# Performance work log

Hardware: AMD Instinct MI355X
Metric: run time of the kernel (lower is better)

The kernel has to match this reference:

```python
import jax, jax.numpy as jnp
import numpy as np

NEG_INF = -9e15  # matches -9000000000000000.0 in torch code
ALPHA = 0.2      # LeakyReLU negative slope


def setup_inputs() -> dict:
    key = jax.random.key(0)
    k1, k2, k3, k4 = jax.random.split(key, 4)
    B, N, Fin, Fout = 8, 2048, 256, 256
    h = jax.random.normal(k1, (B, N, Fin), dtype=jnp.float32)
    adj = jax.random.randint(k2, (B, N, N), 0, 2, dtype=jnp.int32)
    W = jax.random.normal(k3, (Fin, Fout), dtype=jnp.float32) * 0.05
    a = jax.random.normal(k4, (2 * Fout, 1), dtype=jnp.float32) * 0.05
    return {"h": h, "adj": adj, "W": W, "a": a}


def reference(h, adj, W, a):
    # h: [B,N,Fin], adj: [B,N,N], W: [Fin,Fout], a: [2*Fout,1]
    Fout = W.shape[1]
    Wh = jnp.matmul(h, W)                       # [B,N,Fout]
    # Decompose concat-based additive score: e_ij = LReLU(a1.Wh_i + a2.Wh_j)
    a1 = a[:Fout, 0]                            # source-node part
    a2 = a[Fout:, 0]                            # target-node part
    s1 = jnp.einsum('bnf,f->bn', Wh, a1)        # [B,N]
    s2 = jnp.einsum('bnf,f->bn', Wh, a2)        # [B,N]
    e = jax.nn.leaky_relu(s1[:, :, None] + s2[:, None, :], negative_slope=ALPHA)  # [B,N,N]
    attn = jnp.where(adj > 0, e, NEG_INF)
    attn = jax.nn.softmax(attn, axis=2)          # masked softmax over neighbors
    # dropout omitted (deterministic eval-mode reference)
    h_prime = jnp.matmul(attn, Wh)               # [B,N,Fout]
    return h_prime
```

## Files before the change

### kernel.cpp

```cpp
#include <hip/hip_runtime.h>
#include <cstdint>

#define ALPHA 0.2f

constexpr int NB = 8;
constexpr int NN = 2048;
constexpr int NF = 256;

typedef __attribute__((ext_vector_type(8))) short bf16x8;
typedef __attribute__((ext_vector_type(4))) float f32x4;

__device__ __forceinline__ float bf2f(unsigned short u) {
    union { unsigned int i; float f; } v;
    v.i = ((unsigned int)u) << 16;
    return v.f;
}
__device__ __forceinline__ unsigned short f2bf(float f) {
    union { float f; unsigned int i; } v;
    v.f = f;
    v.i += 0x7fffu + ((v.i >> 16) & 1);
    return (unsigned short)(v.i >> 16);
}

__global__ __launch_bounds__(256) void k_wt(const float* __restrict__ W,
                                            unsigned short* __restrict__ WT,
                                            float* __restrict__ s1,
                                            float* __restrict__ s2) {
    const int t = threadIdx.x;
    const int gid = blockIdx.x * 256 + t;
    s1[gid] = 0.f;
    s2[gid] = 0.f;
    const int k = blockIdx.x * 4 + (t >> 6);
    const int f0 = (t & 63) * 4;
    const float4 w = *(const float4*)&W[k * NF + f0];
    WT[(f0 + 0) * NF + k] = f2bf(w.x);
    WT[(f0 + 1) * NF + k] = f2bf(w.y);
    WT[(f0 + 2) * NF + k] = f2bf(w.z);
    WT[(f0 + 3) * NF + k] = f2bf(w.w);
}

__global__ __launch_bounds__(256, 4) void k_wh(const float* __restrict__ h,
                                               const unsigned short* __restrict__ WT,
                                               const float* __restrict__ a,
                                               unsigned short* __restrict__ WhT,
                                               float* __restrict__ s1,
                                               float* __restrict__ s2) {
    __shared__ __align__(16) unsigned short As[64][72];
    __shared__ __align__(16) unsigned short Bs[64][72];
    const int tid = threadIdx.x;
    const int lane = tid & 63;
    const int l16 = lane & 15;
    const int quad = lane >> 4;
    const int wave = tid >> 6;
    const int row0 = (blockIdx.x >> 2) * 64;
    const int col0 = (blockIdx.x & 3) * 64;
    const int bb = row0 >> 11;
    const int n0 = row0 & (NN - 1);
    const int mb = (wave & 1) * 32;
    const int nb = (wave >> 1) * 32;

    f32x4 acc[2][2];
#pragma unroll
    for (int mf = 0; mf < 2; ++mf)
#pragma unroll
        for (int nf = 0; nf < 2; ++nf) acc[mf][nf] = (f32x4){0.f, 0.f, 0.f, 0.f};

    for (int k0 = 0; k0 < NF; k0 += 64) {
#pragma unroll
        for (int it = 0; it < 4; ++it) {
            const int q = tid + it * 256;
            const int r = q >> 4;
            const int k4 = (q & 15) * 4;
            const float4 v = *(const float4*)&h[(size_t)(row0 + r) * NF + k0 + k4];
            ushort4 o;
            o.x = f2bf(v.x); o.y = f2bf(v.y); o.z = f2bf(v.z); o.w = f2bf(v.w);
            *(ushort4*)&As[r][k4] = o;
        }
#pragma unroll
        for (int it = 0; it < 2; ++it) {
            const int q = tid + it * 256;
            const int f = q >> 3;
            const int k8 = (q & 7) * 8;
            *(uint4*)&Bs[f][k8] =
                *(const uint4*)&WT[(size_t)(col0 + f) * NF + k0 + k8];
        }
        __syncthreads();
#pragma unroll
        for (int ks = 0; ks < 64; ks += 32) {
            bf16x8 av[2], bv[2];
#pragma unroll
            for (int mf = 0; mf < 2; ++mf)
                av[mf] = *(const bf16x8*)&As[mb + mf * 16 + l16][ks + quad * 8];
#pragma unroll
            for (int nf = 0; nf < 2; ++nf)
                bv[nf] = *(const bf16x8*)&Bs[nb + nf * 16 + l16][ks + quad * 8];
#pragma unroll
            for (int mf = 0; mf < 2; ++mf)
#pragma unroll
                for (int nf = 0; nf < 2; ++nf)
                    acc[mf][nf] = __builtin_amdgcn_mfma_f32_16x16x32_bf16(
                        av[mf], bv[nf], acc[mf][nf], 0, 0, 0);
        }
        __syncthreads();
    }

#pragma unroll
    for (int mf = 0; mf < 2; ++mf) {
#pragma unroll
        for (int nf = 0; nf < 2; ++nf) {
            const size_t f = col0 + nb + nf * 16 + l16;
            const int nr = n0 + mb + mf * 16 + quad * 4;
            ushort4 o;
            o.x = f2bf(acc[mf][nf][0]);
            o.y = f2bf(acc[mf][nf][1]);
            o.z = f2bf(acc[mf][nf][2]);
            o.w = f2bf(acc[mf][nf][3]);
            *(ushort4*)&WhT[((size_t)bb * NF + f) * NN + nr] = o;
        }
    }

    float a1v[2], a2v[2];
#pragma unroll
    for (int nf = 0; nf < 2; ++nf) {
        const int f = col0 + nb + nf * 16 + l16;
        a1v[nf] = a[f];
        a2v[nf] = a[NF + f];
    }
#pragma unroll
    for (int mf = 0; mf < 2; ++mf) {
#pragma unroll
        for (int r = 0; r < 4; ++r) {
            float p1 = acc[mf][0][r] * a1v[0] + acc[mf][1][r] * a1v[1];
            float p2 = acc[mf][0][r] * a2v[0] + acc[mf][1][r] * a2v[1];
            p1 += __shfl_xor(p1, 1); p2 += __shfl_xor(p2, 1);
            p1 += __shfl_xor(p1, 2); p2 += __shfl_xor(p2, 2);
            p1 += __shfl_xor(p1, 4); p2 += __shfl_xor(p2, 4);
            p1 += __shfl_xor(p1, 8); p2 += __shfl_xor(p2, 8);
            if (l16 == 0) {
                const int n = n0 + mb + mf * 16 + quad * 4 + r;
                atomicAdd(&s1[bb * NN + n], p1);
                atomicAdd(&s2[bb * NN + n], p2);
            }
        }
    }
}

__global__ __launch_bounds__(256, 3) void k_attn(const unsigned short* __restrict__ WhT,
                                                 const int* __restrict__ adj,
                                                 const float* __restrict__ s1g,
                                                 const float* __restrict__ s2g,
                                                 float* __restrict__ out) {
    __shared__ __align__(16) unsigned short WhsT[256][72];
    __shared__ __align__(16) unsigned short Pb[32][72];
    __shared__ float s1_s[32];
    __shared__ float l_s[32];

    const int tid = threadIdx.x;
    const int lane = tid & 63;
    const int l16 = lane & 15;
    const int quad = lane >> 4;
    const int wave = tid >> 6;
    const int bb = blockIdx.x >> 6;
    const int i0 = (blockIdx.x & 63) * 32;

    if (tid < 32) {
        s1_s[tid] = s1g[bb * NN + i0 + tid];
        l_s[tid] = 0.f;
    }
    __syncthreads();

    f32x4 acc[2][4];
#pragma unroll
    for (int m = 0; m < 2; ++m)
#pragma unroll
        for (int nf = 0; nf < 4; ++nf) acc[m][nf] = (f32x4){0.f, 0.f, 0.f, 0.f};

    const size_t whtBase = (size_t)bb * NF * NN;
    const size_t adjBase = (size_t)bb * NN * NN;
    const float* s2b = s2g + bb * NN;

    const int whF = tid >> 3;
    const int whK = (tid & 7) * 8;
    const int pIr = tid >> 4;
    const int pKq = (tid & 15) * 4;

    const unsigned short* whP = &WhT[whtBase + (size_t)whF * NN + whK];
    const int* adjP0 = &adj[adjBase + (size_t)(i0 + pIr) * NN + pKq];
    const int* adjP1 = adjP0 + 16 * NN;
    const float* s2P = &s2b[pKq];

    uint4 w0, w1, w2, w3, w4, w5, w6, w7;
    int4 am0, am1;
    float4 sv0, sv1;

#define LOAD_TILE(J0)                                                         \
    do {                                                                      \
        const int j0_ = (J0);                                                 \
        w0 = *(const uint4*)&whP[(size_t)(0 * 32) * NN + j0_];                \
        w1 = *(const uint4*)&whP[(size_t)(1 * 32) * NN + j0_];                \
        w2 = *(const uint4*)&whP[(size_t)(2 * 32) * NN + j0_];                \
        w3 = *(const uint4*)&whP[(size_t)(3 * 32) * NN + j0_];                \
        w4 = *(const uint4*)&whP[(size_t)(4 * 32) * NN + j0_];                \
        w5 = *(const uint4*)&whP[(size_t)(5 * 32) * NN + j0_];                \
        w6 = *(const uint4*)&whP[(size_t)(6 * 32) * NN + j0_];                \
        w7 = *(const uint4*)&whP[(size_t)(7 * 32) * NN + j0_];                \
        am0 = *(const int4*)&adjP0[j0_];                                      \
        am1 = *(const int4*)&adjP1[j0_];                                      \
        sv0 = *(const float4*)&s2P[j0_];                                      \
        sv1 = sv0;                                                            \
    } while (0)

    LOAD_TILE(0);

    for (int t = 0; t < NN / 64; ++t) {
        *(uint4*)&WhsT[whF + 0 * 32][whK] = w0;
        *(uint4*)&WhsT[whF + 1 * 32][whK] = w1;
        *(uint4*)&WhsT[whF + 2 * 32][whK] = w2;
        *(uint4*)&WhsT[whF + 3 * 32][whK] = w3;
        *(uint4*)&WhsT[whF + 4 * 32][whK] = w4;
        *(uint4*)&WhsT[whF + 5 * 32][whK] = w5;
        *(uint4*)&WhsT[whF + 6 * 32][whK] = w6;
        *(uint4*)&WhsT[whF + 7 * 32][whK] = w7;
#pragma unroll
        for (int it = 0; it < 2; ++it) {
            const int ir = pIr + it * 16;
            const int4 av = it ? am1 : am0;
            const float4 s2v = it ? sv1 : sv0;
            const float s1v = s1_s[ir];
            float x0 = s1v + s2v.x, x1 = s1v + s2v.y;
            float x2 = s1v + s2v.z, x3 = s1v + s2v.w;
            x0 = x0 > 0.f ? x0 : ALPHA * x0;
            x1 = x1 > 0.f ? x1 : ALPHA * x1;
            x2 = x2 > 0.f ? x2 : ALPHA * x2;
            x3 = x3 > 0.f ? x3 : ALPHA * x3;
            const float p0 = av.x > 0 ? __expf(x0) : 0.f;
            const float p1 = av.y > 0 ? __expf(x1) : 0.f;
            const float p2 = av.z > 0 ? __expf(x2) : 0.f;
            const float p3 = av.w > 0 ? __expf(x3) : 0.f;
            uint2 pk;
            pk.x = (unsigned int)f2bf(p0) | ((unsigned int)f2bf(p1) << 16);
            pk.y = (unsigned int)f2bf(p2) | ((unsigned int)f2bf(p3) << 16);
            *(uint2*)&Pb[ir][pKq] = pk;
            float ps = (p0 + p1) + (p2 + p3);
            ps += __shfl_xor(ps, 8);
            ps += __shfl_xor(ps, 4);
            ps += __shfl_xor(ps, 2);
            ps += __shfl_xor(ps, 1);
            if ((tid & 15) == 0) l_s[ir] += ps;
        }
        __syncthreads();
        if (t + 1 < NN / 64) LOAD_TILE((t + 1) * 64);
        const int f0 = wave * 64;
#pragma unroll
        for (int k0 = 0; k0 < 64; k0 += 32) {
            bf16x8 af[2];
#pragma unroll
            for (int m = 0; m < 2; ++m)
                af[m] = *(const bf16x8*)&Pb[m * 16 + l16][k0 + quad * 8];
#pragma unroll
            for (int nf = 0; nf < 4; ++nf) {
                const bf16x8 bfr =
                    *(const bf16x8*)&WhsT[f0 + nf * 16 + l16][k0 + quad * 8];
#pragma unroll
                for (int m = 0; m < 2; ++m)
                    acc[m][nf] = __builtin_amdgcn_mfma_f32_16x16x32_bf16(
                        af[m], bfr, acc[m][nf], 0, 0, 0);
            }
        }
        __syncthreads();
    }
#undef LOAD_TILE

    if (tid < 32) l_s[tid] = 1.0f / l_s[tid];
    __syncthreads();

    const int f0 = wave * 64;
#pragma unroll
    for (int m = 0; m < 2; ++m) {
#pragma unroll
        for (int r = 0; r < 4; ++r) {
            const int row = m * 16 + quad * 4 + r;
            const float inv = l_s[row];
#pragma unroll
            for (int nf = 0; nf < 4; ++nf) {
                out[((size_t)bb * NN + i0 + row) * NF + f0 + nf * 16 + l16] =
                    acc[m][nf][r] * inv;
            }
        }
    }
}

extern "C" void kernel_launch(void* const* d_in, const int* in_sizes, int n_in,
                              void* d_out, int out_size, void* d_ws, size_t ws_size,
                              hipStream_t stream) {
    const float* h = (const float*)d_in[0];
    const int* adj = (const int*)d_in[1];
    const float* W = (const float*)d_in[2];
    const float* a = (const float*)d_in[3];
    float* out = (float*)d_out;

    unsigned short* WhT = (unsigned short*)d_ws;
    float* s1 = (float*)((char*)d_ws + (size_t)NB * NN * NF * sizeof(unsigned short));
    float* s2 = s1 + (size_t)NB * NN;
    unsigned short* WT = (unsigned short*)(s2 + (size_t)NB * NN);

    k_wt<<<dim3(64), dim3(256), 0, stream>>>(W, WT, s1, s2);
    k_wh<<<dim3((NB * NN / 64) * (NF / 64)), dim3(256), 0, stream>>>(h, WT, a, WhT, s1, s2);
    k_attn<<<dim3(NB * (NN / 32)), dim3(256), 0, stream>>>(WhT, adj, s1, s2, out);
}
```

Baseline: 239.2 us.

## Load Wh MFMA operands directly from global into registers, double-buffer adjacency loads

Removes the shared-memory staging tile for the transposed Wh and has each wave load its own B-fragments for the MFMA straight from global memory into registers. Adjacency and s2 loads are double-buffered two tiles ahead, with the loop unrolled by two. This cuts LDS traffic and shared-memory footprint, which may allow more resident blocks. The cost is that Wh reads are no longer shared across waves in a block and are issued as scattered 16-byte loads per lane, and B loads now sit right after the MFMA phase with less latency hiding.

```diff
diff --git a/kernel.cpp b/kernel.cpp
--- a/kernel.cpp
+++ b/kernel.cpp
@@ -150,7 +150,6 @@
                                                  const float* __restrict__ s1g,
                                                  const float* __restrict__ s2g,
                                                  float* __restrict__ out) {
-    __shared__ __align__(16) unsigned short WhsT[256][72];
     __shared__ __align__(16) unsigned short Pb[32][72];
     __shared__ float s1_s[32];
     __shared__ float l_s[32];
@@ -179,97 +178,121 @@
     const size_t adjBase = (size_t)bb * NN * NN;
     const float* s2b = s2g + bb * NN;
 
-    const int whF = tid >> 3;
-    const int whK = (tid & 7) * 8;
     const int pIr = tid >> 4;
     const int pKq = (tid & 15) * 4;
-
-    const unsigned short* whP = &WhT[whtBase + (size_t)whF * NN + whK];
     const int* adjP0 = &adj[adjBase + (size_t)(i0 + pIr) * NN + pKq];
     const int* adjP1 = adjP0 + 16 * NN;
     const float* s2P = &s2b[pKq];
-
-    uint4 w0, w1, w2, w3, w4, w5, w6, w7;
-    int4 am0, am1;
-    float4 sv0, sv1;
-
-#define LOAD_TILE(J0)                                                         \
-    do {                                                                      \
-        const int j0_ = (J0);                                                 \
-        w0 = *(const uint4*)&whP[(size_t)(0 * 32) * NN + j0_];                \
-        w1 = *(const uint4*)&whP[(size_t)(1 * 32) * NN + j0_];                \
-        w2 = *(const uint4*)&whP[(size_t)(2 * 32) * NN + j0_];                \
-        w3 = *(const uint4*)&whP[(size_t)(3 * 32) * NN + j0_];                \
-        w4 = *(const uint4*)&whP[(size_t)(4 * 32) * NN + j0_];                \
-        w5 = *(const uint4*)&whP[(size_t)(5 * 32) * NN + j0_];                \
-        w6 = *(const uint4*)&whP[(size_t)(6 * 32) * NN + j0_];                \
-        w7 = *(const uint4*)&whP[(size_t)(7 * 32) * NN + j0_];                \
-        am0 = *(const int4*)&adjP0[j0_];                                      \
-        am1 = *(const int4*)&adjP1[j0_];                                      \
-        sv0 = *(const float4*)&s2P[j0_];                                      \
-        sv1 = sv0;                                                            \
+    const unsigned short* whW = &WhT[whtBase + (size_t)(wave * 64 + l16) * NN + quad * 8];
+
+    bf16x8 w0, w1, w2, w3, w4, w5, w6, w7;
+    int4 amA0, amA1, amB0, amB1;
+    float4 svA, svB;
+
+#define B_LOAD(J0)                                                    \
+    do {                                                              \
+        const int j_ = (J0);                                          \
+        w0 = *(const bf16x8*)&whW[(size_t)(0 * 16) * NN + j_ + 0];    \
+        w1 = *(const bf16x8*)&whW[(size_t)(0 * 16) * NN + j_ + 32];   \
+        w2 = *(const bf16x8*)&whW[(size_t)(1 * 16) * NN + j_ + 0];    \
+        w3 = *(const bf16x8*)&whW[(size_t)(1 * 16) * NN + j_ + 32];   \
+        w4 = *(const bf16x8*)&whW[(size_t)(2 * 16) * NN + j_ + 0];    \
+        w5 = *(const bf16x8*)&whW[(size_t)(2 * 16) * NN + j_ + 32];   \
+        w6 = *(const bf16x8*)&whW[(size_t)(3 * 16) * NN + j_ + 0];    \
+        w7 = *(const bf16x8*)&whW[(size_t)(3 * 16) * NN + j_ + 32];   \
     } while (0)
 
-    LOAD_TILE(0);
-
-    for (int t = 0; t < NN / 64; ++t) {
-        *(uint4*)&WhsT[whF + 0 * 32][whK] = w0;
-        *(uint4*)&WhsT[whF + 1 * 32][whK] = w1;
-        *(uint4*)&WhsT[whF + 2 * 32][whK] = w2;
-        *(uint4*)&WhsT[whF + 3 * 32][whK] = w3;
-        *(uint4*)&WhsT[whF + 4 * 32][whK] = w4;
-        *(uint4*)&WhsT[whF + 5 * 32][whK] = w5;
-        *(uint4*)&WhsT[whF + 6 * 32][whK] = w6;
-        *(uint4*)&WhsT[whF + 7 * 32][whK] = w7;
-#pragma unroll
-        for (int it = 0; it < 2; ++it) {
-            const int ir = pIr + it * 16;
-            const int4 av = it ? am1 : am0;
-            const float4 s2v = it ? sv1 : sv0;
-            const float s1v = s1_s[ir];
-            float x0 = s1v + s2v.x, x1 = s1v + s2v.y;
-            float x2 = s1v + s2v.z, x3 = s1v + s2v.w;
-            x0 = x0 > 0.f ? x0 : ALPHA * x0;
-            x1 = x1 > 0.f ? x1 : ALPHA * x1;
-            x2 = x2 > 0.f ? x2 : ALPHA * x2;
-            x3 = x3 > 0.f ? x3 : ALPHA * x3;
-            const float p0 = av.x > 0 ? __expf(x0) : 0.f;
-            const float p1 = av.y > 0 ? __expf(x1) : 0.f;
-            const float p2 = av.z > 0 ? __expf(x2) : 0.f;
-            const float p3 = av.w > 0 ? __expf(x3) : 0.f;
-            uint2 pk;
-            pk.x = (unsigned int)f2bf(p0) | ((unsigned int)f2bf(p1) << 16);
-            pk.y = (unsigned int)f2bf(p2) | ((unsigned int)f2bf(p3) << 16);
-            *(uint2*)&Pb[ir][pKq] = pk;
-            float ps = (p0 + p1) + (p2 + p3);
-            ps += __shfl_xor(ps, 8);
-            ps += __shfl_xor(ps, 4);
-            ps += __shfl_xor(ps, 2);
-            ps += __shfl_xor(ps, 1);
-            if ((tid & 15) == 0) l_s[ir] += ps;
-        }
-        __syncthreads();
-        if (t + 1 < NN / 64) LOAD_TILE((t + 1) * 64);
-        const int f0 = wave * 64;
-#pragma unroll
-        for (int k0 = 0; k0 < 64; k0 += 32) {
-            bf16x8 af[2];
-#pragma unroll
-            for (int m = 0; m < 2; ++m)
-                af[m] = *(const bf16x8*)&Pb[m * 16 + l16][k0 + quad * 8];
-#pragma unroll
-            for (int nf = 0; nf < 4; ++nf) {
-                const bf16x8 bfr =
-                    *(const bf16x8*)&WhsT[f0 + nf * 16 + l16][k0 + quad * 8];
-#pragma unroll
-                for (int m = 0; m < 2; ++m)
-                    acc[m][nf] = __builtin_amdgcn_mfma_f32_16x16x32_bf16(
-                        af[m], bfr, acc[m][nf], 0, 0, 0);
-            }
-        }
-        __syncthreads();
-    }
-#undef LOAD_TILE
+#define ADJ_LOAD(AM0, AM1, SV, J0)                                    \
+    do {                                                              \
+        const int j_ = (J0);                                          \
+        AM0 = *(const int4*)&adjP0[j_];                               \
+        AM1 = *(const int4*)&adjP1[j_];                               \
+        SV = *(const float4*)&s2P[j_];                                \
+    } while (0)
+
+#define P_HALF(AV, SV, IR)                                            \
+    do {                                                              \
+        const float s1v = s1_s[IR];                                   \
+        float x0 = s1v + SV.x, x1 = s1v + SV.y;                       \
+        float x2 = s1v + SV.z, x3 = s1v + SV.w;                       \
+        x0 = x0 > 0.f ? x0 : ALPHA * x0;                              \
+        x1 = x1 > 0.f ? x1 : ALPHA * x1;                              \
+        x2 = x2 > 0.f ? x2 : ALPHA * x2;                              \
+        x3 = x3 > 0.f ? x3 : ALPHA * x3;                              \
+        const float p0 = AV.x > 0 ? __expf(x0) : 0.f;                 \
+        const float p1 = AV.y > 0 ? __expf(x1) : 0.f;                 \
+        const float p2 = AV.z > 0 ? __expf(x2) : 0.f;                 \
+        const float p3 = AV.w > 0 ? __expf(x3) : 0.f;                 \
+        uint2 pk;                                                     \
+        pk.x = (unsigned int)f2bf(p0) | ((unsigned int)f2bf(p1) << 16);\
+        pk.y = (unsigned int)f2bf(p2) | ((unsigned int)f2bf(p3) << 16);\
+        *(uint2*)&Pb[IR][pKq] = pk;                                   \
+        float ps = (p0 + p1) + (p2 + p3);                             \
+        ps += __shfl_xor(ps, 8);                                      \
+        ps += __shfl_xor(ps, 4);                                      \
+        ps += __shfl_xor(ps, 2);                                      \
+        ps += __shfl_xor(ps, 1);                                      \
+        if ((tid & 15) == 0) l_s[IR] += ps;                           \
+    } while (0)
+
+#define MFMA_PHASE()                                                  \
+    do {                                                              \
+        bf16x8 af0 = *(const bf16x8*)&Pb[l16][quad * 8];              \
+        bf16x8 af1 = *(const bf16x8*)&Pb[16 + l16][quad * 8];         \
+        acc[0][0] = __builtin_amdgcn_mfma_f32_16x16x32_bf16(af0, w0, acc[0][0], 0, 0, 0); \
+        acc[1][0] = __builtin_amdgcn_mfma_f32_16x16x32_bf16(af1, w0, acc[1][0], 0, 0, 0); \
+        acc[0][1] = __builtin_amdgcn_mfma_f32_16x16x32_bf16(af0, w2, acc[0][1], 0, 0, 0); \
+        acc[1][1] = __builtin_amdgcn_mfma_f32_16x16x32_bf16(af1, w2, acc[1][1], 0, 0, 0); \
+        acc[0][2] = __builtin_amdgcn_mfma_f32_16x16x32_bf16(af0, w4, acc[0][2], 0, 0, 0); \
+        acc[1][2] = __builtin_amdgcn_mfma_f32_16x16x32_bf16(af1, w4, acc[1][2], 0, 0, 0); \
+        acc[0][3] = __builtin_amdgcn_mfma_f32_16x16x32_bf16(af0, w6, acc[0][3], 0, 0, 0); \
+        acc[1][3] = __builtin_amdgcn_mfma_f32_16x16x32_bf16(af1, w6, acc[1][3], 0, 0, 0); \
+        af0 = *(const bf16x8*)&Pb[l16][32 + quad * 8];                \
+        af1 = *(const bf16x8*)&Pb[16 + l16][32 + quad * 8];           \
+        acc[0][0] = __builtin_amdgcn_mfma_f32_16x16x32_bf16(af0, w1, acc[0][0], 0, 0, 0); \
+        acc[1][0] = __builtin_amdgcn_mfma_f32_16x16x32_bf16(af1, w1, acc[1][0], 0, 0, 0); \
+        acc[0][1] = __builtin_amdgcn_mfma_f32_16x16x32_bf16(af0, w3, acc[0][1], 0, 0, 0); \
+        acc[1][1] = __builtin_amdgcn_mfma_f32_16x16x32_bf16(af1, w3, acc[1][1], 0, 0, 0); \
+        acc[0][2] = __builtin_amdgcn_mfma_f32_16x16x32_bf16(af0, w5, acc[0][2], 0, 0, 0); \
+        acc[1][2] = __builtin_amdgcn_mfma_f32_16x16x32_bf16(af1, w5, acc[1][2], 0, 0, 0); \
+        acc[0][3] = __builtin_amdgcn_mfma_f32_16x16x32_bf16(af0, w7, acc[0][3], 0, 0, 0); \
+        acc[1][3] = __builtin_amdgcn_mfma_f32_16x16x32_bf16(af1, w7, acc[1][3], 0, 0, 0); \
+    } while (0)
+
+    constexpr int NT = NN / 64;
+    ADJ_LOAD(amA0, amA1, svA, 0);
+    ADJ_LOAD(amB0, amB1, svB, 64);
+    B_LOAD(0);
+
+    for (int t = 0; t < NT; t += 2) {
+        P_HALF(amA0, svA, pIr);
+        P_HALF(amA1, svA, pIr + 16);
+        __syncthreads();
+        MFMA_PHASE();
+        B_LOAD((t + 1) * 64);
+        {
+            const int j2 = (t + 2 < NT) ? (t + 2) * 64 : 0;
+            ADJ_LOAD(amA0, amA1, svA, j2);
+        }
+        __syncthreads();
+        P_HALF(amB0, svB, pIr);
+        P_HALF(amB1, svB, pIr + 16);
+        __syncthreads();
+        MFMA_PHASE();
+        {
+            const int j1 = (t + 2 < NT) ? (t + 2) * 64 : 0;
+            B_LOAD(j1);
+        }
+        {
+            const int j3 = (t + 3 < NT) ? (t + 3) * 64 : 0;
+            ADJ_LOAD(amB0, amB1, svB, j3);
+        }
+        __syncthreads();
+    }
+#undef B_LOAD
+#undef ADJ_LOAD
+#undef P_HALF
+#undef MFMA_PHASE
 
     if (tid < 32) l_s[tid] = 1.0f / l_s[tid];
     __syncthreads();
```

Result: slower. 257.6 us (+7.7%).
